# Performance work log

Hardware: AMD Instinct MI355X
Metric: run time of the kernel (lower is better)

Reference implementation:

```python
import jax, jax.numpy as jnp
import numpy as np

EPS = 1e-3


def batchnorm(x, gamma, beta):
    # BatchNorm1d in training mode: batch mean and biased variance over dim 0
    mean = jnp.mean(x, axis=0)
    var = jnp.var(x, axis=0)  # biased, matches torch BN normalization
    return (x - mean) * jax.lax.rsqrt(var + EPS) * gamma + beta


def setup_inputs() -> dict:
    key = jax.random.key(0)
    ks = jax.random.split(key, 12)
    N, C_in, C_out, G = 400000, 64, 128, 30000
    points_xyz = jax.random.normal(ks[0], (N, 3), dtype=jnp.float32) * 10.0
    feat_all = jax.random.normal(ks[1], (N, C_in), dtype=jnp.float32)
    unq_inv = jax.random.randint(ks[2], (N,), 0, G, dtype=jnp.int32)
    s_in = 1.0 / np.sqrt(C_in)
    s3 = 1.0 / np.sqrt(3.0)
    return {
        "points_xyz": points_xyz,
        "feat_all": feat_all,
        "unq_inv": unq_inv,
        "W_pre": jax.random.uniform(ks[3], (C_in, C_out), jnp.float32, -s_in, s_in),
        "b_pre": jax.random.uniform(ks[4], (C_out,), jnp.float32, -s_in, s_in),
        "g1": jnp.ones((C_out,), jnp.float32),
        "be1": jnp.zeros((C_out,), jnp.float32),
        "Wp1": jax.random.uniform(ks[5], (3, C_out), jnp.float32, -s3, s3),
        "bp1": jax.random.uniform(ks[6], (C_out,), jnp.float32, -s3, s3),
        "Wp2": jax.random.uniform(ks[7], (3, C_out), jnp.float32, -s3, s3),
        "bp2": jax.random.uniform(ks[8], (C_out,), jnp.float32, -s3, s3),
        "g2": jnp.ones((C_out,), jnp.float32),
        "be2": jnp.zeros((C_out,), jnp.float32),
        "num_segments": 30000,
    }


def reference(points_xyz, feat_all, unq_inv, W_pre, b_pre, g1, be1,
              Wp1, bp1, Wp2, bp2, g2, be2, num_segments):
    p = jnp.floor(points_xyz)                       # [N, 3]
    feat = batchnorm(feat_all @ W_pre + b_pre, g1, be1)  # [N, C_out]
    pw1 = p @ Wp1 + bp1                             # [N, C_out]
    pw2 = p @ Wp2 + bp2                             # [N, C_out]
    feat_weight = pw1 * feat                        # [N, C_out]
    feat_add = jax.ops.segment_sum(feat_weight, unq_inv,
                                   num_segments=num_segments)  # [G, C_out]
    feat_add = feat_add[unq_inv]                    # gather back: [N, C_out]
    out = pw2 * feat - feat_add
    out = jax.nn.relu(batchnorm(out, g2, be2))
    return out
```

## Files before the change

### kernel.cpp

```cpp
#include <hip/hip_runtime.h>
#include <hip/hip_bf16.h>

typedef unsigned int u32;
typedef unsigned short u16;
typedef __attribute__((ext_vector_type(8))) short short8;
typedef __attribute__((ext_vector_type(4))) float floatx4;

#define COUT 128
#define GSEG 30000
#define BN_EPS 1e-3f

__device__ __forceinline__ u32 f2bf(float x) {
    u32 u = __float_as_uint(x);
    return (u + 0x7fffu + ((u >> 16) & 1u)) >> 16;
}
__device__ __forceinline__ float bf2f(u32 b) { return __uint_as_float(b << 16); }

__device__ __forceinline__ void unpack8(uint4 v, float* f) {
    f[0] = __uint_as_float(v.x << 16); f[1] = __uint_as_float(v.x & 0xffff0000u);
    f[2] = __uint_as_float(v.y << 16); f[3] = __uint_as_float(v.y & 0xffff0000u);
    f[4] = __uint_as_float(v.z << 16); f[5] = __uint_as_float(v.z & 0xffff0000u);
    f[6] = __uint_as_float(v.w << 16); f[7] = __uint_as_float(v.w & 0xffff0000u);
}

__global__ __launch_bounds__(512) void k_gemm_bn1(
    const float* __restrict__ A, const float* __restrict__ W,
    const float* __restrict__ bias, const int* __restrict__ unq, int* __restrict__ cnt,
    u16* __restrict__ lin, float* __restrict__ sum1, float* __restrict__ sumsq1, int n)
{
    __shared__ union {
        struct { u16 ahi[128 * 72]; u16 alo[128 * 72]; u16 whi[128 * 72]; u16 wlo[128 * 72]; } s;
        u16 pack[128 * 136];
    } sm;
    __shared__ float sSum[128], sSq[128];

    const int t = threadIdx.x;
    const int row0 = blockIdx.x * 128;
    if (t < 128) { sSum[t] = 0.f; sSq[t] = 0.f; }

    if (t < 128 && row0 + t < n) atomicAdd(&cnt[unq[row0 + t]], 1);

#pragma unroll
    for (int j = 0; j < 4; j++) {
        int f = t + j * 512;
        int row = f >> 4, k0 = (f & 15) << 2;
        float4 v = make_float4(0.f, 0.f, 0.f, 0.f);
        if (row0 + row < n) v = *(const float4*)&A[(size_t)(row0 + row) * 64 + k0];
        float vv[4] = {v.x, v.y, v.z, v.w};
        u32 hb[4], lb[4];
#pragma unroll
        for (int i = 0; i < 4; i++) {
            hb[i] = f2bf(vv[i]);
            lb[i] = f2bf(vv[i] - bf2f(hb[i]));
        }
        uint2 ph = make_uint2(hb[0] | (hb[1] << 16), hb[2] | (hb[3] << 16));
        uint2 pl = make_uint2(lb[0] | (lb[1] << 16), lb[2] | (lb[3] << 16));
        *(uint2*)&sm.s.ahi[row * 72 + k0] = ph;
        *(uint2*)&sm.s.alo[row * 72 + k0] = pl;
    }
#pragma unroll
    for (int j = 0; j < 4; j++) {
        int f = t + j * 512;
        int k = f >> 5, c0 = (f & 31) << 2;
        float4 w4 = *(const float4*)&W[k * 128 + c0];
        float wv[4] = {w4.x, w4.y, w4.z, w4.w};
#pragma unroll
        for (int i = 0; i < 4; i++) {
            u32 hb = f2bf(wv[i]);
            float lo = wv[i] - bf2f(hb);
            sm.s.whi[(c0 + i) * 72 + k] = (u16)hb;
            sm.s.wlo[(c0 + i) * 72 + k] = (u16)f2bf(lo);
        }
    }
    __syncthreads();

    const int lane = t & 63, wv = t >> 6;
    const int r = lane & 15, q = lane >> 4;
    const int rw0 = wv * 16;

    short8 arh[2], arl[2];
#pragma unroll
    for (int ks = 0; ks < 2; ks++) {
        arh[ks] = *(const short8*)&sm.s.ahi[(rw0 + r) * 72 + ks * 32 + q * 8];
        arl[ks] = *(const short8*)&sm.s.alo[(rw0 + r) * 72 + ks * 32 + q * 8];
    }

    floatx4 acc[8];
#pragma unroll
    for (int ct = 0; ct < 8; ct++) acc[ct] = (floatx4){0.f, 0.f, 0.f, 0.f};

#pragma unroll
    for (int ct = 0; ct < 8; ct++) {
#pragma unroll
        for (int ks = 0; ks < 2; ks++) {
            short8 wh = *(const short8*)&sm.s.whi[(ct * 16 + r) * 72 + ks * 32 + q * 8];
            short8 wl = *(const short8*)&sm.s.wlo[(ct * 16 + r) * 72 + ks * 32 + q * 8];
            acc[ct] = __builtin_amdgcn_mfma_f32_16x16x32_bf16(arh[ks], wh, acc[ct], 0, 0, 0);
            acc[ct] = __builtin_amdgcn_mfma_f32_16x16x32_bf16(arl[ks], wh, acc[ct], 0, 0, 0);
            acc[ct] = __builtin_amdgcn_mfma_f32_16x16x32_bf16(arh[ks], wl, acc[ct], 0, 0, 0);
        }
    }
    __syncthreads();

#pragma unroll
    for (int ct = 0; ct < 8; ct++) {
        int c = ct * 16 + r;
        float bv = bias[c];
        float ssum = 0.f, ssq = 0.f;
#pragma unroll
        for (int i = 0; i < 4; i++) {
            int lrow = rw0 + q * 4 + i;
            float v = acc[ct][i] + bv;
            if (row0 + lrow >= n) v = 0.f;
            ssum += v; ssq += v * v;
            sm.pack[lrow * 136 + c] = (u16)f2bf(v);
        }
        ssum += __shfl_xor(ssum, 16, 64); ssq += __shfl_xor(ssq, 16, 64);
        ssum += __shfl_xor(ssum, 32, 64); ssq += __shfl_xor(ssq, 32, 64);
        if (lane < 16) { atomicAdd(&sSum[c], ssum); atomicAdd(&sSq[c], ssq); }
    }
    __syncthreads();

#pragma unroll
    for (int j = 0; j < 4; j++) {
        int f = t + j * 512;
        int row = f >> 4, c0 = (f & 15) << 3;
        if (row0 + row < n) {
            uint4 v = *(const uint4*)&sm.pack[row * 136 + c0];
            *(uint4*)(lin + (size_t)(row0 + row) * 128 + c0) = v;
        }
    }
    if (t < 128) { atomicAdd(&sum1[t], sSum[t]); atomicAdd(&sumsq1[t], sSq[t]); }
}

__global__ void k_fin(const float* __restrict__ sum, const float* __restrict__ sumsq,
                      const float* __restrict__ g, const float* __restrict__ be,
                      float* __restrict__ scale, float* __restrict__ shift, float inv_n)
{
    int c = threadIdx.x;
    float mean = sum[c] * inv_n;
    float var = sumsq[c] * inv_n - mean * mean;
    float sc = g[c] * rsqrtf(var + BN_EPS);
    scale[c] = sc;
    shift[c] = be[c] - mean * sc;
}

__global__ __launch_bounds__(1024) void k_scan(const int* __restrict__ cnt,
                                               int* __restrict__ offs,
                                               int* __restrict__ cursor)
{
    __shared__ int wsum[16];
    int t = threadIdx.x, lane = t & 63, wv = t >> 6;
    int base = t * 32;
    int v[32];
    int s = 0;
    if (base + 32 <= GSEG) {
        const int4* cp = (const int4*)(cnt + base);
#pragma unroll
        for (int j = 0; j < 8; j++) {
            int4 q = cp[j];
            v[j * 4 + 0] = q.x; v[j * 4 + 1] = q.y; v[j * 4 + 2] = q.z; v[j * 4 + 3] = q.w;
            s += q.x + q.y + q.z + q.w;
        }
    } else {
#pragma unroll
        for (int j = 0; j < 32; j++) {
            int idx = base + j;
            int x = (idx < GSEG) ? cnt[idx] : 0;
            v[j] = x; s += x;
        }
    }
    int x = s;
#pragma unroll
    for (int d = 1; d < 64; d <<= 1) {
        int u = __shfl_up(x, d, 64);
        if (lane >= d) x += u;
    }
    if (lane == 63) wsum[wv] = x;
    __syncthreads();
    if (t < 16) {
        int w = wsum[t];
#pragma unroll
        for (int d = 1; d < 16; d <<= 1) {
            int u = __shfl_up(w, d, 16);
            if (t >= d) w += u;
        }
        wsum[t] = w;
    }
    __syncthreads();
    int run = (wv ? wsum[wv - 1] : 0) + (x - s);
#pragma unroll
    for (int j = 0; j < 32; j++) {
        int idx = base + j;
        if (idx < GSEG) { offs[idx] = run; cursor[idx] = run; }
        run += v[j];
    }
    if (t == 1023) offs[GSEG] = wsum[15];
}

__global__ __launch_bounds__(256) void k_scatter_idx(const int* __restrict__ unq,
                                                     int* __restrict__ cursor,
                                                     int* __restrict__ order, int n)
{
    int i = blockIdx.x * 256 + threadIdx.x;
    if (i < n) {
        int pos = atomicAdd(&cursor[unq[i]], 1);
        order[pos] = i;
    }
}

__global__ __launch_bounds__(256) void k_segsum(
    const u16* __restrict__ lin, const float* __restrict__ xyz,
    const int* __restrict__ order, const int* __restrict__ offs,
    const float* __restrict__ scale1, const float* __restrict__ shift1,
    const float* __restrict__ Wp1, const float* __restrict__ bp1,
    const float* __restrict__ Wp2, const float* __restrict__ bp2,
    float* __restrict__ feat_add, float* __restrict__ sum2, float* __restrict__ sumsq2,
    int nseg)
{
    __shared__ float sSum[128], sSq[128];
    const int t = threadIdx.x;
    if (t < 128) { sSum[t] = 0.f; sSq[t] = 0.f; }
    __syncthreads();
    const int wave = t >> 6, lane = t & 63;
    const int c = lane * 2;
    const float wa0x = Wp1[c],     wa0y = Wp1[128 + c],     wa0z = Wp1[256 + c],     ba0 = bp1[c];
    const float wa1x = Wp1[c + 1], wa1y = Wp1[128 + c + 1], wa1z = Wp1[256 + c + 1], ba1 = bp1[c + 1];
    const float wb0x = Wp2[c],     wb0y = Wp2[128 + c],     wb0z = Wp2[256 + c],     bb0 = bp2[c];
    const float wb1x = Wp2[c + 1], wb1y = Wp2[128 + c + 1], wb1z = Wp2[256 + c + 1], bb1 = bp2[c + 1];
    const float sc0 = scale1[c], sh0 = shift1[c];
    const float sc1 = scale1[c + 1], sh1 = shift1[c + 1];
    float rs0 = 0.f, rs1 = 0.f, rq0 = 0.f, rq1 = 0.f;
    const int stride = gridDim.x * 4;
    for (int s = blockIdx.x * 4 + wave; s < nseg; s += stride) {
        const int beg = offs[s], end = offs[s + 1];
        const int m = end - beg;
        int rowv = 0; float fxv = 0.f, fyv = 0.f, fzv = 0.f;
        if (lane < m) {
            rowv = order[beg + lane];
            fxv = floorf(xyz[rowv * 3]);
            fyv = floorf(xyz[rowv * 3 + 1]);
            fzv = floorf(xyz[rowv * 3 + 2]);
        }
        float acc0 = 0.f, acc1 = 0.f, p10 = 0.f, p11 = 0.f, p20 = 0.f, p21 = 0.f;
        const int mm = m < 64 ? m : 64;
        for (int j = 0; j < mm; j++) {
            int row = __shfl(rowv, j, 64);
            float px = __shfl(fxv, j, 64);
            float py = __shfl(fyv, j, 64);
            float pz = __shfl(fzv, j, 64);
            u32 l2 = *(const u32*)(lin + (size_t)row * 128 + c);
            float fe0 = fmaf(__uint_as_float(l2 << 16), sc0, sh0);
            float fe1 = fmaf(__uint_as_float(l2 & 0xffff0000u), sc1, sh1);
            float pa0 = fmaf(px, wa0x, fmaf(py, wa0y, fmaf(pz, wa0z, ba0)));
            float pa1 = fmaf(px, wa1x, fmaf(py, wa1y, fmaf(pz, wa1z, ba1)));
            float pb0 = fmaf(px, wb0x, fmaf(py, wb0y, fmaf(pz, wb0z, bb0)));
            float pb1 = fmaf(px, wb1x, fmaf(py, wb1y, fmaf(pz, wb1z, bb1)));
            acc0 = fmaf(pa0, fe0, acc0);
            acc1 = fmaf(pa1, fe1, acc1);
            float t0 = pb0 * fe0, t1 = pb1 * fe1;
            p10 += t0; p11 += t1;
            p20 = fmaf(t0, t0, p20); p21 = fmaf(t1, t1, p21);
        }
        for (int j = 64; j < m; j++) {
            int row = order[beg + j];
            float px = floorf(xyz[row * 3]);
            float py = floorf(xyz[row * 3 + 1]);
            float pz = floorf(xyz[row * 3 + 2]);
            u32 l2 = *(const u32*)(lin + (size_t)row * 128 + c);
            float fe0 = fmaf(__uint_as_float(l2 << 16), sc0, sh0);
            float fe1 = fmaf(__uint_as_float(l2 & 0xffff0000u), sc1, sh1);
            float pa0 = fmaf(px, wa0x, fmaf(py, wa0y, fmaf(pz, wa0z, ba0)));
            float pa1 = fmaf(px, wa1x, fmaf(py, wa1y, fmaf(pz, wa1z, ba1)));
            float pb0 = fmaf(px, wb0x, fmaf(py, wb0y, fmaf(pz, wb0z, bb0)));
            float pb1 = fmaf(px, wb1x, fmaf(py, wb1y, fmaf(pz, wb1z, bb1)));
            acc0 = fmaf(pa0, fe0, acc0);
            acc1 = fmaf(pa1, fe1, acc1);
            float t0 = pb0 * fe0, t1 = pb1 * fe1;
            p10 += t0; p11 += t1;
            p20 = fmaf(t0, t0, p20); p21 = fmaf(t1, t1, p21);
        }
        float2 st; st.x = acc0; st.y = acc1;
        *(float2*)(feat_add + (size_t)s * 128 + c) = st;
        float fm = (float)m;
        rs0 += p10 - fm * acc0;
        rs1 += p11 - fm * acc1;
        rq0 += fmaf(fm * acc0, acc0, p20 - 2.f * acc0 * p10);
        rq1 += fmaf(fm * acc1, acc1, p21 - 2.f * acc1 * p11);
    }
    atomicAdd(&sSum[c], rs0); atomicAdd(&sSum[c + 1], rs1);
    atomicAdd(&sSq[c], rq0);  atomicAdd(&sSq[c + 1], rq1);
    __syncthreads();
    if (t < 128) { atomicAdd(&sum2[t], sSum[t]); atomicAdd(&sumsq2[t], sSq[t]); }
}

__global__ __launch_bounds__(256) void k_final(
    const u16* __restrict__ lin, const float* __restrict__ xyz, const int* __restrict__ unq,
    const float* __restrict__ scale1, const float* __restrict__ shift1,
    const float* __restrict__ Wp2, const float* __restrict__ bp2,
    const float* __restrict__ feat_add,
    const float* __restrict__ scale2, const float* __restrict__ shift2,
    float* __restrict__ out, int n)
{
    __shared__ float sS[128], sH[128], sW3[384], sB[128], sS2[128], sH2[128];
    int t = threadIdx.x;
    if (t < 128) {
        sS[t] = scale1[t]; sH[t] = shift1[t]; sB[t] = bp2[t];
        sW3[t] = Wp2[t]; sW3[128 + t] = Wp2[128 + t]; sW3[256 + t] = Wp2[256 + t];
        sS2[t] = scale2[t]; sH2[t] = shift2[t];
    }
    __syncthreads();
    int row = blockIdx.x * 16 + (t >> 4);
    if (row >= n) return;
    int c0 = (t & 15) * 8;
    uint4 l8 = *(const uint4*)(lin + (size_t)row * 128 + c0);
    float f[8];
    unpack8(l8, f);
    float px = floorf(xyz[row * 3 + 0]);
    float py = floorf(xyz[row * 3 + 1]);
    float pz = floorf(xyz[row * 3 + 2]);
    int g = unq[row];
    const float4* fa = (const float4*)(feat_add + (size_t)g * 128 + c0);
    float4 fa0 = fa[0], fa1 = fa[1];
    float fav[8] = {fa0.x, fa0.y, fa0.z, fa0.w, fa1.x, fa1.y, fa1.z, fa1.w};
    float o[8];
#pragma unroll
    for (int j = 0; j < 8; j++) {
        int c = c0 + j;
        float fe = fmaf(f[j], sS[c], sH[c]);
        float pw = fmaf(px, sW3[c], fmaf(py, sW3[128 + c], fmaf(pz, sW3[256 + c], sB[c])));
        float v = pw * fe - fav[j];
        v = fmaf(v, sS2[c], sH2[c]);
        o[j] = v > 0.f ? v : 0.f;
    }
    float4 s0, s1;
    s0.x = o[0]; s0.y = o[1]; s0.z = o[2]; s0.w = o[3];
    s1.x = o[4]; s1.y = o[5]; s1.z = o[6]; s1.w = o[7];
    float* op = out + (size_t)row * 128 + c0;
    *(float4*)op = s0;
    *(float4*)(op + 4) = s1;
}

extern "C" void kernel_launch(void* const* d_in, const int* in_sizes, int n_in,
                              void* d_out, int out_size, void* d_ws, size_t ws_size,
                              hipStream_t stream)
{
    const float* xyz      = (const float*)d_in[0];
    const float* feat_all = (const float*)d_in[1];
    const int*   unq      = (const int*)d_in[2];
    const float* W_pre    = (const float*)d_in[3];
    const float* b_pre    = (const float*)d_in[4];
    const float* g1       = (const float*)d_in[5];
    const float* be1      = (const float*)d_in[6];
    const float* Wp1      = (const float*)d_in[7];
    const float* bp1      = (const float*)d_in[8];
    const float* Wp2      = (const float*)d_in[9];
    const float* bp2      = (const float*)d_in[10];
    const float* g2       = (const float*)d_in[11];
    const float* be2      = (const float*)d_in[12];
    (void)n_in; (void)out_size; (void)ws_size;

    const int n = in_sizes[0] / 3;

    char* ws = (char*)d_ws;
    float* stats  = (float*)ws;
    float* sum1   = stats;       float* sumsq1 = stats + 128;
    float* sum2   = stats + 256; float* sumsq2 = stats + 384;
    float* scale1 = stats + 512; float* shift1 = stats + 640;
    float* scale2 = stats + 768; float* shift2 = stats + 896;
    int*   cnt      = (int*)(ws + 4096);
    int*   offs     = (int*)(ws + 124160);
    int*   cursor   = (int*)(ws + 244224);
    int*   order    = (int*)(ws + 364288);
    float* feat_add = (float*)(ws + 1964544);
    u16*   lin      = (u16*)(ws + 17324544);

    hipMemsetAsync(d_ws, 0, 124160, stream);

    k_gemm_bn1<<<(n + 127) / 128, 512, 0, stream>>>(feat_all, W_pre, b_pre, unq, cnt,
                                                    lin, sum1, sumsq1, n);
    k_fin<<<1, 128, 0, stream>>>(sum1, sumsq1, g1, be1, scale1, shift1, 1.0f / n);

    k_scan<<<1, 1024, 0, stream>>>(cnt, offs, cursor);
    k_scatter_idx<<<(n + 255) / 256, 256, 0, stream>>>(unq, cursor, order, n);
    k_segsum<<<1876, 256, 0, stream>>>(lin, xyz, order, offs, scale1, shift1,
                                       Wp1, bp1, Wp2, bp2, feat_add, sum2, sumsq2, GSEG);
    k_fin<<<1, 128, 0, stream>>>(sum2, sumsq2, g2, be2, scale2, shift2, 1.0f / n);
    k_final<<<(n + 15) / 16, 256, 0, stream>>>(lin, xyz, unq, scale1, shift1, Wp2, bp2,
                                               feat_add, scale2, shift2, (float*)d_out, n);
}
```

Measured before the change: 585.3 us.

## Precompute bf16 hi/lo weight split once and load GEMM operands directly to registers

Adds a one-block prep kernel that splits W_pre into transposed bf16 hi/lo halves in workspace once. The GEMM kernel then reads the weight fragments straight from global memory (L2-resident) and loads each A row's fragment directly into registers, so the shared-memory staging and its barrier are gone. This removes the per-block weight conversion and the LDS round trip, and shrinks LDS use, which may let more blocks run per CU. The trade-off is uncoalesced 16-byte global reads for A and W fragments in place of staged LDS reads, plus one extra kernel launch.

```diff
diff --git a/kernel.cpp b/kernel.cpp
--- a/kernel.cpp
+++ b/kernel.cpp
@@ -23,15 +23,26 @@
     f[6] = __uint_as_float(v.w << 16); f[7] = __uint_as_float(v.w & 0xffff0000u);
 }
 
+__global__ __launch_bounds__(512) void k_prep_w(
+    const float* __restrict__ W, u16* __restrict__ wt_hi, u16* __restrict__ wt_lo)
+{
+    int t = threadIdx.x;
+    for (int f = t; f < 8192; f += 512) {
+        int k = f >> 7, c = f & 127;
+        float w = W[f];
+        u32 hb = f2bf(w);
+        float lo = w - bf2f(hb);
+        wt_hi[c * 64 + k] = (u16)hb;
+        wt_lo[c * 64 + k] = (u16)f2bf(lo);
+    }
+}
+
 __global__ __launch_bounds__(512) void k_gemm_bn1(
-    const float* __restrict__ A, const float* __restrict__ W,
+    const float* __restrict__ A, const u16* __restrict__ wt_hi, const u16* __restrict__ wt_lo,
     const float* __restrict__ bias, const int* __restrict__ unq, int* __restrict__ cnt,
     u16* __restrict__ lin, float* __restrict__ sum1, float* __restrict__ sumsq1, int n)
 {
-    __shared__ union {
-        struct { u16 ahi[128 * 72]; u16 alo[128 * 72]; u16 whi[128 * 72]; u16 wlo[128 * 72]; } s;
-        u16 pack[128 * 136];
-    } sm;
+    __shared__ u16 pack[128 * 136];
     __shared__ float sSum[128], sSq[128];
 
     const int t = threadIdx.x;
@@ -40,49 +51,29 @@
 
     if (t < 128 && row0 + t < n) atomicAdd(&cnt[unq[row0 + t]], 1);
 
-#pragma unroll
-    for (int j = 0; j < 4; j++) {
-        int f = t + j * 512;
-        int row = f >> 4, k0 = (f & 15) << 2;
-        float4 v = make_float4(0.f, 0.f, 0.f, 0.f);
-        if (row0 + row < n) v = *(const float4*)&A[(size_t)(row0 + row) * 64 + k0];
-        float vv[4] = {v.x, v.y, v.z, v.w};
-        u32 hb[4], lb[4];
-#pragma unroll
-        for (int i = 0; i < 4; i++) {
-            hb[i] = f2bf(vv[i]);
-            lb[i] = f2bf(vv[i] - bf2f(hb[i]));
-        }
-        uint2 ph = make_uint2(hb[0] | (hb[1] << 16), hb[2] | (hb[3] << 16));
-        uint2 pl = make_uint2(lb[0] | (lb[1] << 16), lb[2] | (lb[3] << 16));
-        *(uint2*)&sm.s.ahi[row * 72 + k0] = ph;
-        *(uint2*)&sm.s.alo[row * 72 + k0] = pl;
-    }
-#pragma unroll
-    for (int j = 0; j < 4; j++) {
-        int f = t + j * 512;
-        int k = f >> 5, c0 = (f & 31) << 2;
-        float4 w4 = *(const float4*)&W[k * 128 + c0];
-        float wv[4] = {w4.x, w4.y, w4.z, w4.w};
-#pragma unroll
-        for (int i = 0; i < 4; i++) {
-            u32 hb = f2bf(wv[i]);
-            float lo = wv[i] - bf2f(hb);
-            sm.s.whi[(c0 + i) * 72 + k] = (u16)hb;
-            sm.s.wlo[(c0 + i) * 72 + k] = (u16)f2bf(lo);
-        }
-    }
-    __syncthreads();
-
     const int lane = t & 63, wv = t >> 6;
     const int r = lane & 15, q = lane >> 4;
     const int rw0 = wv * 16;
+    const int row_a = row0 + rw0 + r;
+    const bool ok = row_a < n;
 
     short8 arh[2], arl[2];
+    const float* ap = A + (size_t)row_a * 64;
 #pragma unroll
     for (int ks = 0; ks < 2; ks++) {
-        arh[ks] = *(const short8*)&sm.s.ahi[(rw0 + r) * 72 + ks * 32 + q * 8];
-        arl[ks] = *(const short8*)&sm.s.alo[(rw0 + r) * 72 + ks * 32 + q * 8];
+        float4 v0 = make_float4(0.f, 0.f, 0.f, 0.f), v1 = v0;
+        if (ok) {
+            v0 = *(const float4*)(ap + ks * 32 + q * 8);
+            v1 = *(const float4*)(ap + ks * 32 + q * 8 + 4);
+        }
+        float vv[8] = {v0.x, v0.y, v0.z, v0.w, v1.x, v1.y, v1.z, v1.w};
+#pragma unroll
+        for (int i = 0; i < 8; i++) {
+            u32 hb = f2bf(vv[i]);
+            float lo = vv[i] - bf2f(hb);
+            arh[ks][i] = (short)(u16)hb;
+            arl[ks][i] = (short)(u16)f2bf(lo);
+        }
     }
 
     floatx4 acc[8];
@@ -91,10 +82,12 @@
 
 #pragma unroll
     for (int ct = 0; ct < 8; ct++) {
+        const u16* whp = wt_hi + (ct * 16 + r) * 64 + q * 8;
+        const u16* wlp = wt_lo + (ct * 16 + r) * 64 + q * 8;
 #pragma unroll
         for (int ks = 0; ks < 2; ks++) {
-            short8 wh = *(const short8*)&sm.s.whi[(ct * 16 + r) * 72 + ks * 32 + q * 8];
-            short8 wl = *(const short8*)&sm.s.wlo[(ct * 16 + r) * 72 + ks * 32 + q * 8];
+            short8 wh = *(const short8*)(whp + ks * 32);
+            short8 wl = *(const short8*)(wlp + ks * 32);
             acc[ct] = __builtin_amdgcn_mfma_f32_16x16x32_bf16(arh[ks], wh, acc[ct], 0, 0, 0);
             acc[ct] = __builtin_amdgcn_mfma_f32_16x16x32_bf16(arl[ks], wh, acc[ct], 0, 0, 0);
             acc[ct] = __builtin_amdgcn_mfma_f32_16x16x32_bf16(arh[ks], wl, acc[ct], 0, 0, 0);
@@ -113,7 +106,7 @@
             float v = acc[ct][i] + bv;
             if (row0 + lrow >= n) v = 0.f;
             ssum += v; ssq += v * v;
-            sm.pack[lrow * 136 + c] = (u16)f2bf(v);
+            pack[lrow * 136 + c] = (u16)f2bf(v);
         }
         ssum += __shfl_xor(ssum, 16, 64); ssq += __shfl_xor(ssq, 16, 64);
         ssum += __shfl_xor(ssum, 32, 64); ssq += __shfl_xor(ssq, 32, 64);
@@ -126,7 +119,7 @@
         int f = t + j * 512;
         int row = f >> 4, c0 = (f & 15) << 3;
         if (row0 + row < n) {
-            uint4 v = *(const uint4*)&sm.pack[row * 136 + c0];
+            uint4 v = *(const uint4*)&pack[row * 136 + c0];
             *(uint4*)(lin + (size_t)(row0 + row) * 128 + c0) = v;
         }
     }
@@ -372,12 +365,15 @@
     int*   offs     = (int*)(ws + 124160);
     int*   cursor   = (int*)(ws + 244224);
     int*   order    = (int*)(ws + 364288);
+    u16*   wt_hi    = (u16*)(ws + 1964544 - 32768);
+    u16*   wt_lo    = (u16*)(ws + 1964544 - 16384);
     float* feat_add = (float*)(ws + 1964544);
     u16*   lin      = (u16*)(ws + 17324544);
 
     hipMemsetAsync(d_ws, 0, 124160, stream);
 
-    k_gemm_bn1<<<(n + 127) / 128, 512, 0, stream>>>(feat_all, W_pre, b_pre, unq, cnt,
+    k_prep_w<<<1, 512, 0, stream>>>(W_pre, wt_hi, wt_lo);
+    k_gemm_bn1<<<(n + 127) / 128, 512, 0, stream>>>(feat_all, wt_hi, wt_lo, b_pre, unq, cnt,
                                                     lin, sum1, sumsq1, n);
     k_fin<<<1, 128, 0, stream>>>(sum1, sumsq1, g1, be1, scale1, shift1, 1.0f / n);
 
```

Measured after the change: 614.2 us. +4.9%, slower.
